# Kernel tuning notes

Hardware: AMD Instinct MI355X
Metric: run time of the kernel (lower is better)

The kernel has to match this reference:

```python
import jax, jax.numpy as jnp
import numpy as np

D_MODEL, D_K, D_V, HEADS = 512, 8, 8, 6
EPS = 1e-5


def setup_inputs() -> dict:
    key = jax.random.key(0)
    ks = jax.random.split(key, 16)
    B, S = 16, 1024
    inp = {
        'q_input': jax.random.normal(ks[0], (B, S, D_MODEL), jnp.float32),
        'k_input': jax.random.normal(ks[1], (B, S, D_MODEL), jnp.float32),
        'v_input': jax.random.normal(ks[2], (B, S, D_MODEL), jnp.float32),
        'mask': jax.random.randint(ks[3], (B, S, S), 0, 2).astype(bool),
        'Wq': jax.random.normal(ks[4], (D_MODEL, D_K * HEADS), jnp.float32) * 0.04,
        'bq': jax.random.normal(ks[5], (D_K * HEADS,), jnp.float32) * 0.02,
        'Wk': jax.random.normal(ks[6], (D_MODEL, D_K * HEADS), jnp.float32) * 0.04,
        'bk': jax.random.normal(ks[7], (D_K * HEADS,), jnp.float32) * 0.02,
        'Wv': jax.random.normal(ks[8], (D_MODEL, D_V * HEADS), jnp.float32) * 0.04,
        'bv': jax.random.normal(ks[9], (D_V * HEADS,), jnp.float32) * 0.02,
        'Wo': jax.random.normal(ks[10], (HEADS * D_K, D_MODEL), jnp.float32) * 0.1,
        'bo': jax.random.normal(ks[11], (D_MODEL,), jnp.float32) * 0.02,
        'ln_w': 1.0 + jax.random.normal(ks[12], (D_MODEL,), jnp.float32) * 0.02,
        'ln_b': jax.random.normal(ks[13], (D_MODEL,), jnp.float32) * 0.02,
    }
    return inp


def reference(q_input, k_input, v_input, mask, Wq, bq, Wk, bk, Wv, bv, Wo, bo, ln_w, ln_b):
    B, S, _ = q_input.shape
    # projections -> [B, H, S, d]
    q_s = (q_input @ Wq + bq).reshape(B, S, HEADS, D_K).transpose(0, 2, 1, 3)
    k_s = (k_input @ Wk + bk).reshape(B, S, HEADS, D_K).transpose(0, 2, 1, 3)
    v_s = (v_input @ Wv + bv).reshape(B, S, HEADS, D_V).transpose(0, 2, 1, 3)
    # scaled dot-product with masked_fill(mask, 1e-9) as in the original (fills VALUE, not -inf)
    scores = jnp.einsum('bhqd,bhkd->bhqk', q_s, k_s) / np.sqrt(D_K).astype(np.float32)
    scores = jnp.where(mask[:, None, :, :], jnp.float32(1e-9), scores)
    attn = jax.nn.softmax(scores, axis=-1)
    out = jnp.einsum('bhqk,bhkd->bhqd', attn, v_s)  # [B,H,S,d_v]
    out = out.transpose(0, 2, 1, 3).reshape(B, S, HEADS * D_K)
    out = out @ Wo + bo
    x = q_input + out  # residual
    mu = jnp.mean(x, axis=-1, keepdims=True)
    var = jnp.var(x, axis=-1, keepdims=True)
    return (x - mu) * jax.lax.rsqrt(var + EPS) * ln_w + ln_b
```

## Files before the change

### kernel.cpp

```cpp
#include <hip/hip_runtime.h>

constexpr int B = 16;
constexpr int S = 1024;
constexpr int DM = 512;
constexpr int H = 6;
constexpr int DK = 8;
constexpr int NJ = H * DK;
constexpr int BS = B * S;

typedef __attribute__((ext_vector_type(8))) short bf16x8;
typedef __attribute__((ext_vector_type(4))) float floatx4;

#define LOG2E 1.4426950408889634f
#define QSCALE (0.35355339059327373f * LOG2E)
#define MASKVAL (1e-9f * LOG2E)

__device__ inline ushort f2bf(float f) {
  unsigned int u = __builtin_bit_cast(unsigned int, f);
  return (ushort)((u + 0x7FFFu + ((u >> 16) & 1u)) >> 16);
}

__global__ __launch_bounds__(256) void maskbits_kernel(
    const int* __restrict__ mask, unsigned long long* __restrict__ bits) {
  int wave = threadIdx.x >> 6, lane = threadIdx.x & 63;
  int row = blockIdx.x * 4 + wave;
  const int* mrow = mask + (size_t)row * S;
  unsigned long long* brow = bits + (size_t)row * 16;
#pragma unroll
  for (int c = 0; c < 16; c++) {
    int v = mrow[c * 64 + lane];
    unsigned long long bal = __ballot(v != 0);
    if (lane == 0) brow[c] = bal;
  }
}

__global__ __launch_bounds__(256) void wprep_kernel(
    const float* __restrict__ Wq, const float* __restrict__ Wk,
    const float* __restrict__ Wv, ushort* __restrict__ Wt) {
  int m = blockIdx.x;
  const float* W = (m == 0) ? Wq : (m == 1) ? Wk : Wv;
  ushort* dst = Wt + (size_t)m * NJ * DM;
  for (int e = threadIdx.x; e < DM * NJ; e += 256) {
    int k = e / NJ, n = e - k * NJ;
    dst[n * DM + k] = f2bf(W[e]);
  }
}

__global__ __launch_bounds__(256) void proj_kernel(
    const float* __restrict__ q_in, const float* __restrict__ k_in,
    const float* __restrict__ v_in, const ushort* __restrict__ Wt,
    const float* __restrict__ bq, const float* __restrict__ bk,
    const float* __restrict__ bv,
    ushort* __restrict__ Qo, ushort* __restrict__ Ko, ushort* __restrict__ Vo) {
  int m = blockIdx.y;
  const float* x    = (m == 0) ? q_in : (m == 1) ? k_in : v_in;
  const float* bias = (m == 0) ? bq   : (m == 1) ? bk   : bv;
  ushort* out       = (m == 0) ? Qo   : (m == 1) ? Ko   : Vo;
  float oscale      = (m == 0) ? QSCALE : 1.0f;
  const ushort* Wg  = Wt + (size_t)m * NJ * DM;

  constexpr int LDK = 264;
  __shared__ ushort Xs[64 * LDK];
  __shared__ ushort Ws[NJ * LDK];

  int t = threadIdx.x;
  int r0 = blockIdx.x * 64;
  int wave = t >> 6, lane = t & 63;
  int mrow = lane & 15, quad = lane >> 4;

  floatx4 acc0 = {0.f, 0.f, 0.f, 0.f};
  floatx4 acc1 = {0.f, 0.f, 0.f, 0.f};
  floatx4 acc2 = {0.f, 0.f, 0.f, 0.f};

#pragma unroll 1
  for (int p = 0; p < 2; p++) {
    int k0 = p * 256;
    __syncthreads();
#pragma unroll
    for (int i = 0; i < 16; i++) {
      int f = t + i * 256;
      int r = f >> 6;
      int c = (f & 63) * 4;
      float4 g = *(const float4*)&x[(size_t)(r0 + r) * DM + k0 + c];
      ushort4 hh = {f2bf(g.x), f2bf(g.y), f2bf(g.z), f2bf(g.w)};
      *(ushort4*)&Xs[r * LDK + c] = hh;
    }
#pragma unroll
    for (int i = 0; i < 12; i++) {
      int f = t + i * 256;
      int n = f >> 6;
      int c = (f & 63) * 4;
      *(ushort4*)&Ws[n * LDK + c] = *(const ushort4*)&Wg[(size_t)n * DM + k0 + c];
    }
    __syncthreads();
#pragma unroll
    for (int kc = 0; kc < 8; kc++) {
      int koff = kc * 32 + quad * 8;
      bf16x8 a  = *(const bf16x8*)&Xs[(wave * 16 + mrow) * LDK + koff];
      bf16x8 b0 = *(const bf16x8*)&Ws[(0  + mrow) * LDK + koff];
      bf16x8 b1 = *(const bf16x8*)&Ws[(16 + mrow) * LDK + koff];
      bf16x8 b2 = *(const bf16x8*)&Ws[(32 + mrow) * LDK + koff];
      acc0 = __builtin_amdgcn_mfma_f32_16x16x32_bf16(a, b0, acc0, 0, 0, 0);
      acc1 = __builtin_amdgcn_mfma_f32_16x16x32_bf16(a, b1, acc1, 0, 0, 0);
      acc2 = __builtin_amdgcn_mfma_f32_16x16x32_bf16(a, b2, acc2, 0, 0, 0);
    }
  }

  int baseR = r0 + wave * 16 + quad * 4;
#pragma unroll
  for (int j = 0; j < 3; j++) {
    floatx4 a = (j == 0) ? acc0 : (j == 1) ? acc1 : acc2;
    int n = j * 16 + mrow;
    float bn = bias[n];
    int h = n >> 3, d = n & 7;
#pragma unroll
    for (int r = 0; r < 4; r++) {
      int R = baseR + r;
      int b = R >> 10, s = R & 1023;
      out[(((size_t)(b * H + h)) * S + s) * 8 + d] = f2bf((a[r] + bn) * oscale);
    }
  }
}

__global__ __launch_bounds__(256) void attn_kernel(
    const ushort* __restrict__ Qg, const ushort* __restrict__ Kg,
    const ushort* __restrict__ Vg, const unsigned long long* __restrict__ bits,
    float* __restrict__ A) {
  int bh = blockIdx.x >> 4;
  int qt = blockIdx.x & 15;
  int b = bh / H, h = bh % H;
  int q0 = qt * 64;

  __shared__ ushort Ks[1024 * 8];
  __shared__ ushort Vt[9 * 1032];
  __shared__ unsigned long long Mw[64 * 16];
  __shared__ uint Pb[4][2][16 * 20];

  int t = threadIdx.x;
  int wave = t >> 6, lane = t & 63;
  int quad = lane >> 4, n16 = lane & 15;

  const ushort* Kbase = Kg + (size_t)bh * S * 8;
  const ushort* Vbase = Vg + (size_t)bh * S * 8;
  const unsigned long long* Bbase = bits + ((size_t)(b * S + q0)) * 16;

#pragma unroll
  for (int i = 0; i < 4; i++) {
    int e = t + i * 256;
    *(uint4*)&Ks[e * 8] = *(const uint4*)&Kbase[e * 8];
  }
#pragma unroll
  for (int i = 0; i < 8; i++) {
    int e = t + i * 256;
    int key = e >> 1, db = (e & 1) << 2;
    ushort4 v = *(const ushort4*)&Vbase[key * 8 + db];
    int g = (key & ~31) + 2 * (key & 15) + ((key >> 4) & 1);
    Vt[(db + 0) * 1032 + g] = v.x;
    Vt[(db + 1) * 1032 + g] = v.y;
    Vt[(db + 2) * 1032 + g] = v.z;
    Vt[(db + 3) * 1032 + g] = v.w;
  }
#pragma unroll
  for (int i = 0; i < 4; i++) Vt[8 * 1032 + t + i * 256] = 0x3F80;
#pragma unroll
  for (int i = 0; i < 4; i++) Mw[t + i * 256] = Bbase[t + i * 256];
  __syncthreads();

  bf16x8 aq = {0, 0, 0, 0, 0, 0, 0, 0};
  if (quad == 0)
    aq = *(const bf16x8*)&Qg[((size_t)bh * S + q0 + wave * 16 + n16) * 8];

  floatx4 acc = {0.f, 0.f, 0.f, 0.f};
  const floatx4 zero = {0.f, 0.f, 0.f, 0.f};

#pragma unroll 2
  for (int c = 0; c < 32; c++) {
    bf16x8 bk0 = *(const bf16x8*)&Ks[(c * 32 + n16) * 8];
    bf16x8 bk1 = *(const bf16x8*)&Ks[(c * 32 + 16 + n16) * 8];
    floatx4 sc0 = __builtin_amdgcn_mfma_f32_16x16x32_bf16(aq, bk0, zero, 0, 0, 0);
    floatx4 sc1 = __builtin_amdgcn_mfma_f32_16x16x32_bf16(aq, bk1, zero, 0, 0, 0);

    int basebit = (c & 1) * 32;
    int wi = c >> 1;
    uint* prow = &Pb[wave][c & 1][0];
#pragma unroll
    for (int r = 0; r < 4; r++) {
      unsigned long long mw = Mw[(wave * 16 + quad * 4 + r) * 16 + wi];
      float s0 = ((mw >> (basebit + n16)) & 1ull) ? MASKVAL : sc0[r];
      float s1 = ((mw >> (basebit + 16 + n16)) & 1ull) ? MASKVAL : sc1[r];
      float p0 = exp2f(fminf(s0, 80.f));
      float p1 = exp2f(fminf(s1, 80.f));
      uint pw = (uint)f2bf(p0) | ((uint)f2bf(p1) << 16);
      prow[(quad * 4 + r) * 20 + n16] = pw;
    }

    bf16x8 ap = *(const bf16x8*)((const ushort*)prow + n16 * 40 + quad * 8);
    int dd = (n16 < 9) ? n16 : 8;
    bf16x8 bv = *(const bf16x8*)&Vt[dd * 1032 + c * 32 + quad * 8];
    acc = __builtin_amdgcn_mfma_f32_16x16x32_bf16(ap, bv, acc, 0, 0, 0);
  }

#pragma unroll
  for (int r = 0; r < 4; r++) {
    float dnm = __shfl(acc[r], (lane & 48) | 8, 64);
    if (n16 < 8) {
      int qg = q0 + wave * 16 + quad * 4 + r;
      A[((size_t)(b * S + qg)) * NJ + h * 8 + n16] = acc[r] / dnm;
    }
  }
}

__global__ __launch_bounds__(256) void out_ln_kernel(
    const float* __restrict__ A, const float* __restrict__ Wo,
    const float* __restrict__ bo, const float* __restrict__ qin,
    const float* __restrict__ lnw, const float* __restrict__ lnb,
    float* __restrict__ out) {
  int r0 = blockIdx.x * 8;
  int t = threadIdx.x;
  __shared__ float As[8 * NJ];
#pragma unroll
  for (int i = t; i < 8 * NJ; i += 256) As[i] = A[(size_t)r0 * NJ + i];
  __syncthreads();

  int c0 = t, c1 = t + 256;
  float acc0[8], acc1[8];
#pragma unroll
  for (int r = 0; r < 8; r++) { acc0[r] = 0.f; acc1[r] = 0.f; }

#pragma unroll 4
  for (int j = 0; j < NJ; j++) {
    float w0 = Wo[(size_t)j * DM + c0];
    float w1 = Wo[(size_t)j * DM + c1];
#pragma unroll
    for (int r = 0; r < 8; r++) {
      float a = As[r * NJ + j];
      acc0[r] += a * w0;
      acc1[r] += a * w1;
    }
  }

  float b0 = bo[c0], b1 = bo[c1];
  float y0[8], y1[8], ssum[8], sq[8];
#pragma unroll
  for (int r = 0; r < 8; r++) {
    y0[r] = acc0[r] + b0 + qin[(size_t)(r0 + r) * DM + c0];
    y1[r] = acc1[r] + b1 + qin[(size_t)(r0 + r) * DM + c1];
    ssum[r] = y0[r] + y1[r];
    sq[r] = y0[r] * y0[r] + y1[r] * y1[r];
  }

  int wave = t >> 6, lane = t & 63;
  __shared__ float reds[4][8], redq[4][8];
#pragma unroll
  for (int r = 0; r < 8; r++) {
    float s = ssum[r], qq = sq[r];
#pragma unroll
    for (int off = 32; off > 0; off >>= 1) {
      s += __shfl_xor(s, off, 64);
      qq += __shfl_xor(qq, off, 64);
    }
    if (lane == 0) { reds[wave][r] = s; redq[wave][r] = qq; }
  }
  __syncthreads();

  float lw0 = lnw[c0], lw1 = lnw[c1], lb0 = lnb[c0], lb1 = lnb[c1];
#pragma unroll
  for (int r = 0; r < 8; r++) {
    float s = (reds[0][r] + reds[1][r]) + (reds[2][r] + reds[3][r]);
    float qq = (redq[0][r] + redq[1][r]) + (redq[2][r] + redq[3][r]);
    float mu = s * (1.f / 512.f);
    float var = qq * (1.f / 512.f) - mu * mu;
    float rstd = rsqrtf(var + 1e-5f);
    out[(size_t)(r0 + r) * DM + c0] = (y0[r] - mu) * rstd * lw0 + lb0;
    out[(size_t)(r0 + r) * DM + c1] = (y1[r] - mu) * rstd * lw1 + lb1;
  }
}

extern "C" void kernel_launch(void* const* d_in, const int* in_sizes, int n_in,
                              void* d_out, int out_size, void* d_ws,
                              size_t ws_size, hipStream_t stream) {
  const float* q_in = (const float*)d_in[0];
  const float* k_in = (const float*)d_in[1];
  const float* v_in = (const float*)d_in[2];
  const int* mask = (const int*)d_in[3];
  const float* Wq = (const float*)d_in[4];
  const float* bq = (const float*)d_in[5];
  const float* Wk = (const float*)d_in[6];
  const float* bk = (const float*)d_in[7];
  const float* Wv = (const float*)d_in[8];
  const float* bv = (const float*)d_in[9];
  const float* Wo = (const float*)d_in[10];
  const float* bo = (const float*)d_in[11];
  const float* lnw = (const float*)d_in[12];
  const float* lnb = (const float*)d_in[13];
  float* out = (float*)d_out;

  constexpr size_t QKV = (size_t)B * H * S * DK;
  ushort* base = (ushort*)d_ws;
  ushort* Qw = base;
  ushort* Kw = base + QKV;
  ushort* Vw = base + 2 * QKV;
  float* Aw = (float*)(base + 3 * QKV);
  unsigned long long* bits = (unsigned long long*)(Aw + (size_t)BS * NJ);
  ushort* Wt = (ushort*)(bits + (size_t)BS * 16);

  maskbits_kernel<<<BS / 4, 256, 0, stream>>>(mask, bits);
  wprep_kernel<<<3, 256, 0, stream>>>(Wq, Wk, Wv, Wt);
  proj_kernel<<<dim3(BS / 64, 3), 256, 0, stream>>>(
      q_in, k_in, v_in, Wt, bq, bk, bv, Qw, Kw, Vw);
  attn_kernel<<<(B * H * S) / 64, 256, 0, stream>>>(Qw, Kw, Vw, bits, Aw);
  out_ln_kernel<<<BS / 8, 256, 0, stream>>>(Aw, Wo, bo, q_in, lnw, lnb, out);
}
```

Measured before the change: 346.7 us.

## Pre-block projection weights for MFMA and load X directly into registers

The weight prep kernel now writes Wq/Wk/Wv in a k-chunked, MFMA-fragment-friendly bf16 layout. The projection kernel copies the whole blocked weight into LDS once, then streams X straight from global memory into registers with bf16 conversion. This drops the X staging through LDS and the per-pass barriers. In exchange each lane issues strided global float4 loads across rows, which coalesce less well than the old staged copy.

```diff
diff --git a/kernel.cpp b/kernel.cpp
--- a/kernel.cpp
+++ b/kernel.cpp
@@ -7,6 +7,7 @@
 constexpr int DK = 8;
 constexpr int NJ = H * DK;
 constexpr int BS = B * S;
+constexpr int WB_ELEMS = 16 * NJ * 32;
 
 typedef __attribute__((ext_vector_type(8))) short bf16x8;
 typedef __attribute__((ext_vector_type(4))) float floatx4;
@@ -36,19 +37,22 @@
 
 __global__ __launch_bounds__(256) void wprep_kernel(
     const float* __restrict__ Wq, const float* __restrict__ Wk,
-    const float* __restrict__ Wv, ushort* __restrict__ Wt) {
+    const float* __restrict__ Wv, ushort* __restrict__ Wb) {
   int m = blockIdx.x;
   const float* W = (m == 0) ? Wq : (m == 1) ? Wk : Wv;
-  ushort* dst = Wt + (size_t)m * NJ * DM;
-  for (int e = threadIdx.x; e < DM * NJ; e += 256) {
-    int k = e / NJ, n = e - k * NJ;
-    dst[n * DM + k] = f2bf(W[e]);
+  ushort* dst = Wb + (size_t)m * WB_ELEMS;
+  for (int e = threadIdx.x; e < WB_ELEMS; e += 256) {
+    int kc = e >> 11;
+    kc = e / 1536;
+    int rem = e - kc * 1536;
+    int n = rem >> 5, kj = rem & 31;
+    dst[e] = f2bf(W[(size_t)(kc * 32 + kj) * NJ + n]);
   }
 }
 
 __global__ __launch_bounds__(256) void proj_kernel(
     const float* __restrict__ q_in, const float* __restrict__ k_in,
-    const float* __restrict__ v_in, const ushort* __restrict__ Wt,
+    const float* __restrict__ v_in, const ushort* __restrict__ Wb,
     const float* __restrict__ bq, const float* __restrict__ bk,
     const float* __restrict__ bv,
     ushort* __restrict__ Qo, ushort* __restrict__ Ko, ushort* __restrict__ Vo) {
@@ -57,60 +61,52 @@
   const float* bias = (m == 0) ? bq   : (m == 1) ? bk   : bv;
   ushort* out       = (m == 0) ? Qo   : (m == 1) ? Ko   : Vo;
   float oscale      = (m == 0) ? QSCALE : 1.0f;
-  const ushort* Wg  = Wt + (size_t)m * NJ * DM;
-
-  constexpr int LDK = 264;
-  __shared__ ushort Xs[64 * LDK];
-  __shared__ ushort Ws[NJ * LDK];
+  const ushort* Wg  = Wb + (size_t)m * WB_ELEMS;
+
+  __shared__ ushort Wl[WB_ELEMS];
 
   int t = threadIdx.x;
+  {
+    const uint4* src = (const uint4*)Wg;
+    uint4* dst = (uint4*)Wl;
+#pragma unroll
+    for (int i = 0; i < 12; i++) dst[t + i * 256] = src[t + i * 256];
+  }
+
   int r0 = blockIdx.x * 64;
   int wave = t >> 6, lane = t & 63;
-  int mrow = lane & 15, quad = lane >> 4;
+  int n16 = lane & 15, quad = lane >> 4;
+  const float* xrow = x + (size_t)(r0 + wave * 16 + n16) * DM + quad * 8;
 
   floatx4 acc0 = {0.f, 0.f, 0.f, 0.f};
   floatx4 acc1 = {0.f, 0.f, 0.f, 0.f};
   floatx4 acc2 = {0.f, 0.f, 0.f, 0.f};
 
-#pragma unroll 1
-  for (int p = 0; p < 2; p++) {
-    int k0 = p * 256;
-    __syncthreads();
-#pragma unroll
-    for (int i = 0; i < 16; i++) {
-      int f = t + i * 256;
-      int r = f >> 6;
-      int c = (f & 63) * 4;
-      float4 g = *(const float4*)&x[(size_t)(r0 + r) * DM + k0 + c];
-      ushort4 hh = {f2bf(g.x), f2bf(g.y), f2bf(g.z), f2bf(g.w)};
-      *(ushort4*)&Xs[r * LDK + c] = hh;
-    }
-#pragma unroll
-    for (int i = 0; i < 12; i++) {
-      int f = t + i * 256;
-      int n = f >> 6;
-      int c = (f & 63) * 4;
-      *(ushort4*)&Ws[n * LDK + c] = *(const ushort4*)&Wg[(size_t)n * DM + k0 + c];
-    }
-    __syncthreads();
-#pragma unroll
-    for (int kc = 0; kc < 8; kc++) {
-      int koff = kc * 32 + quad * 8;
-      bf16x8 a  = *(const bf16x8*)&Xs[(wave * 16 + mrow) * LDK + koff];
-      bf16x8 b0 = *(const bf16x8*)&Ws[(0  + mrow) * LDK + koff];
-      bf16x8 b1 = *(const bf16x8*)&Ws[(16 + mrow) * LDK + koff];
-      bf16x8 b2 = *(const bf16x8*)&Ws[(32 + mrow) * LDK + koff];
-      acc0 = __builtin_amdgcn_mfma_f32_16x16x32_bf16(a, b0, acc0, 0, 0, 0);
-      acc1 = __builtin_amdgcn_mfma_f32_16x16x32_bf16(a, b1, acc1, 0, 0, 0);
-      acc2 = __builtin_amdgcn_mfma_f32_16x16x32_bf16(a, b2, acc2, 0, 0, 0);
-    }
+  __syncthreads();
+
+#pragma unroll 4
+  for (int kc = 0; kc < 16; kc++) {
+    float4 xa = *(const float4*)(xrow + kc * 32);
+    float4 xb = *(const float4*)(xrow + kc * 32 + 4);
+    bf16x8 a;
+    a[0] = (short)f2bf(xa.x); a[1] = (short)f2bf(xa.y);
+    a[2] = (short)f2bf(xa.z); a[3] = (short)f2bf(xa.w);
+    a[4] = (short)f2bf(xb.x); a[5] = (short)f2bf(xb.y);
+    a[6] = (short)f2bf(xb.z); a[7] = (short)f2bf(xb.w);
+    const ushort* wbase = &Wl[(kc * 48 + n16) * 32 + quad * 8];
+    bf16x8 b0 = *(const bf16x8*)(wbase);
+    bf16x8 b1 = *(const bf16x8*)(wbase + 16 * 32);
+    bf16x8 b2 = *(const bf16x8*)(wbase + 32 * 32);
+    acc0 = __builtin_amdgcn_mfma_f32_16x16x32_bf16(a, b0, acc0, 0, 0, 0);
+    acc1 = __builtin_amdgcn_mfma_f32_16x16x32_bf16(a, b1, acc1, 0, 0, 0);
+    acc2 = __builtin_amdgcn_mfma_f32_16x16x32_bf16(a, b2, acc2, 0, 0, 0);
   }
 
   int baseR = r0 + wave * 16 + quad * 4;
 #pragma unroll
   for (int j = 0; j < 3; j++) {
     floatx4 a = (j == 0) ? acc0 : (j == 1) ? acc1 : acc2;
-    int n = j * 16 + mrow;
+    int n = j * 16 + n16;
     float bn = bias[n];
     int h = n >> 3, d = n & 7;
 #pragma unroll
@@ -302,12 +298,12 @@
   ushort* Vw = base + 2 * QKV;
   float* Aw = (float*)(base + 3 * QKV);
   unsigned long long* bits = (unsigned long long*)(Aw + (size_t)BS * NJ);
-  ushort* Wt = (ushort*)(bits + (size_t)BS * 16);
+  ushort* Wb = (ushort*)(bits + (size_t)BS * 16);
 
   maskbits_kernel<<<BS / 4, 256, 0, stream>>>(mask, bits);
-  wprep_kernel<<<3, 256, 0, stream>>>(Wq, Wk, Wv, Wt);
+  wprep_kernel<<<3, 256, 0, stream>>>(Wq, Wk, Wv, Wb);
   proj_kernel<<<dim3(BS / 64, 3), 256, 0, stream>>>(
-      q_in, k_in, v_in, Wt, bq, bk, bv, Qw, Kw, Vw);
+      q_in, k_in, v_in, Wb, bq, bk, bv, Qw, Kw, Vw);
   attn_kernel<<<(B * H * S) / 64, 256, 0, stream>>>(Qw, Kw, Vw, bits, Aw);
   out_ln_kernel<<<BS / 8, 256, 0, stream>>>(Aw, Wo, bo, q_in, lnw, lnb, out);
 }
```

Measured after the change: 316.6 us. 8.7% less time.
